# Kernel optimization log

Hardware: AMD Instinct MI355X
Metric: run time of the kernel (lower is better)

The kernel has to match this reference:

```python
import jax, jax.numpy as jnp
import numpy as np

D = 16       # data dimension
M = 64       # hidden width
ALPHA0 = 1.0 # alpha[0]
H_RES = 1.0  # ResNet step h = 1/(n_layers-1), n_layers=2


def _antideriv_tanh(x):
    # log(exp(x)+exp(-x)), numerically stable
    return jnp.abs(x) + jnp.log1p(jnp.exp(-2.0 * jnp.abs(x)))


def _dtanh(x):
    t = jnp.tanh(x)
    return 1.0 - t * t


def grad_and_hessian_trace(s, w, A, b, K0, b0, K1, b1):
    """OT-Flow analytic grad of Phi and trace of Hessian (w.r.t. first d coords).
    s: (n, d+1) = [x; t]. n_layers=2 -> one residual layer, h=1."""
    d = s.shape[1] - 1
    opening = s @ K0.T + b0                         # (n, m)
    u0 = _antideriv_tanh(opening)                   # (n, m)
    feat1 = u0 @ K1.T + b1                          # (n, m)
    tanhopen = jnp.tanh(opening)                    # (n, m)
    # backward pass for gradient: z1 = w + h K1^T (tanh(feat1) * w)
    z1 = w + H_RES * (jnp.tanh(feat1) * w) @ K1     # (n, m)
    z0 = (tanhopen * z1) @ K0                       # (n, d+1)
    symA = A.T @ A                                  # (d+1, d+1)
    grad = z0 + s @ symA + b                        # (n, d+1)
    # Hessian trace: opening-layer term
    Kopen = K0[:, :d]                               # (m, d)
    trH = (_dtanh(opening) * z1) @ jnp.sum(Kopen**2, axis=1)   # (n,)
    # forward-propagated Jacobian of u0 w.r.t. x: (n, m, d)
    Jac = tanhopen[:, :, None] * Kopen[None, :, :]
    KJ = jnp.einsum('ij,njd->nid', K1, Jac)         # (n, m, d)
    t1 = jnp.einsum('nm,nmd->n', _dtanh(feat1) * w, KJ**2)
    trH = trH + H_RES * t1 + jnp.sum(A[:, :d] ** 2)  # + trace(symA[:d,:d])
    return grad, trH


def odefun(z, t, w, A, b, K0, b0, K1, b1):
    n = z.shape[0]
    x = z[:, :D]
    s = jnp.concatenate([x, jnp.full((n, 1), t, dtype=z.dtype)], axis=1)
    gradPhi, trH = grad_and_hessian_trace(s, w, A, b, K0, b0, K1, b1)
    dx = -(1.0 / ALPHA0) * gradPhi[:, :D]
    dl = -(1.0 / ALPHA0) * trH[:, None]
    dv = 0.5 * jnp.sum(dx * dx, axis=1, keepdims=True)
    dr = jnp.abs(-gradPhi[:, -1:] + ALPHA0 * dv)
    return jnp.concatenate([dx, dl, dv, dr], axis=1)


def step_rk4(f, z, t0, t1):
    h = t1 - t0
    z0 = z
    K = h * f(z0, t0)
    z = z0 + K / 6.0
    K = h * f(z0 + 0.5 * K, t0 + 0.5 * h)
    z = z + K / 3.0
    K = h * f(z0 + 0.5 * K, t0 + 0.5 * h)
    z = z + K / 3.0
    K = h * f(z0 + K, t0 + h)
    z = z + K / 6.0
    return z


def setup_inputs() -> dict:
    key = jax.random.key(0)
    ks = jax.random.split(key, 8)
    n = 32768
    dp1 = D + 1
    x = jax.random.normal(ks[0], (n, D), dtype=jnp.float32)
    w = jax.random.normal(ks[1], (M,), dtype=jnp.float32) / np.sqrt(M)
    A = 0.1 * jax.random.normal(ks[2], (10, dp1), dtype=jnp.float32)
    b = 0.1 * jax.random.normal(ks[3], (dp1,), dtype=jnp.float32)
    K0 = jax.random.normal(ks[4], (M, dp1), dtype=jnp.float32) / np.sqrt(dp1)
    b0 = 0.1 * jax.random.normal(ks[5], (M,), dtype=jnp.float32)
    K1 = jax.random.normal(ks[6], (M, M), dtype=jnp.float32) / np.sqrt(M)
    b1 = 0.1 * jax.random.normal(ks[7], (M,), dtype=jnp.float32)
    return {"x": x, "w": w, "A": A, "b": b, "K0": K0, "b0": b0,
            "K1": K1, "b1": b1, "nt": 8}


def reference(x, w, A, b, K0, b0, K1, b1, nt):
    f = lambda z, t: odefun(z, t, w, A, b, K0, b0, K1, b1)
    h = 1.0 / nt
    z = jnp.concatenate([x, jnp.zeros((x.shape[0], 3), x.dtype)], axis=1)
    for k in range(nt):  # nt is a static python int
        z = step_rk4(f, z, k * h, (k + 1) * h)
    # unpack: (x_latent, log_det, transport_cost, hjb_violation)
    return z[:, :D], z[:, D], z[:, D + 1], z[:, D + 2]
```

## Files before the change

### kernel.cpp

```cpp
#include <hip/hip_runtime.h>
#include <math.h>

typedef __attribute__((ext_vector_type(8))) short bf16x8;
typedef __attribute__((ext_vector_type(4))) float f32x4;
typedef __attribute__((ext_vector_type(2))) float f32x2;
typedef __attribute__((ext_vector_type(4))) unsigned u32x4;

union B8 { bf16x8 v; unsigned u[4]; u32x4 q; };

__device__ __forceinline__ unsigned pk2(float lo, float hi) {
  unsigned r;
  asm("v_cvt_pk_bf16_f32 %0, %1, %2" : "=v"(r) : "v"(lo), "v"(hi));
  return r;
}
__device__ __forceinline__ f32x2 pkmul(f32x2 a, f32x2 b) {
  f32x2 r;
  asm("v_pk_mul_f32 %0, %1, %2" : "=v"(r) : "v"(a), "v"(b));
  return r;
}
__device__ __forceinline__ float rcpf(float x) { return __builtin_amdgcn_rcpf(x); }
__device__ __forceinline__ void ldsfence() { asm volatile("s_waitcnt lgkmcnt(0)" ::: "memory"); }

#define MFMA __builtin_amdgcn_mfma_f32_16x16x32_bf16

__global__ void otflow_prep(const float* __restrict__ K0g,
                            const float* __restrict__ Ag,
                            float* __restrict__ ws) {
  __shared__ float Als[170];
  int tid = threadIdx.x;
  for (int idx = tid; idx < 1024; idx += 256) {
    int m = idx >> 4, d = idx & 15;
    ws[idx] = K0g[m * 17 + d];
  }
  if (tid < 170) Als[tid] = Ag[tid];
  if (tid < 64) {
    float s = 0.f;
    for (int d = 0; d < 16; ++d) { float v = K0g[tid * 17 + d]; s += v * v; }
    ws[1320 + tid] = s;
  }
  __syncthreads();
  for (int idx = tid; idx < 289; idx += 256) {
    int j = idx / 17, k2 = idx % 17;
    float s = 0.f;
#pragma unroll
    for (int r = 0; r < 10; ++r) s += Als[r * 17 + j] * Als[r * 17 + k2];
    ws[1024 + idx] = s;
  }
  __syncthreads();
  if (tid == 0) {
    float s = 0.f;
    for (int r = 0; r < 10; ++r)
      for (int j = 0; j < 16; ++j) { float v = Als[r * 17 + j]; s += v * v; }
    ws[1313] = s;
  }
}

__global__ __launch_bounds__(64, 2) void otflow_main(
    const float* __restrict__ xg, const float* __restrict__ wg,
    const float* __restrict__ bg, const float* __restrict__ K0g,
    const float* __restrict__ b0g, const float* __restrict__ K1g,
    const float* __restrict__ b1g, const int* __restrict__ ntg,
    const float* __restrict__ ws, float* __restrict__ out, int n) {
  __shared__ __align__(16) float csh[16 * 68];
  __shared__ __align__(16) float qsh[16 * 68];
  __shared__ __align__(16) unsigned Xu[16 * 36];
  __shared__ __align__(16) float tsh[16 * 20];
  __shared__ __align__(16) float b0s[64], tcs[64], b1s[64], wss[64], k0qs[64];
  __shared__ __align__(16) float scol[20];

  const int lane = threadIdx.x;
  const int lr = lane & 15;
  const int lg = lane >> 4;

  b0s[lane] = b0g[lane];
  tcs[lane] = K0g[lane * 17 + 16];
  b1s[lane] = b1g[lane];
  wss[lane] = wg[lane];
  k0qs[lane] = ws[1320 + lane];
  if (lane < 17) scol[lane] = ws[1024 + lane * 17 + 16];
  if (lane == 17) scol[17] = bg[16];

  const float sumA2 = ws[1313];

  B8 aK0[4], aK0L[4];
#pragma unroll
  for (int mi = 0; mi < 4; ++mi) {
    B8 th, tl;
#pragma unroll
    for (int jj = 0; jj < 4; ++jj) {
      float e0 = K0g[(mi * 16 + lr) * 17 + (lg & 1) * 8 + jj * 2];
      float e1 = K0g[(mi * 16 + lr) * 17 + (lg & 1) * 8 + jj * 2 + 1];
      unsigned hh = pk2(e0, e1);
      th.u[jj] = hh;
      float l0 = e0 - __uint_as_float(hh << 16);
      float l1 = e1 - __uint_as_float(hh & 0xffff0000u);
      tl.u[jj] = pk2(l0, l1);
    }
    aK0[mi] = th; aK0L[mi] = tl;
  }
  B8 aK1[8];
#pragma unroll
  for (int mi = 0; mi < 4; ++mi)
#pragma unroll
    for (int kb = 0; kb < 2; ++kb) {
      const float* pp = K1g + (mi * 16 + lr) * 64 + kb * 32 + lg * 8;
      float4 q0 = *(const float4*)pp;
      float4 q1 = *(const float4*)(pp + 4);
      B8 t;
      t.u[0] = pk2(q0.x, q0.y); t.u[1] = pk2(q0.z, q0.w);
      t.u[2] = pk2(q1.x, q1.y); t.u[3] = pk2(q1.z, q1.w);
      aK1[mi * 2 + kb] = t;
    }
  B8 aK1T[8];
#pragma unroll
  for (int mi = 0; mi < 4; ++mi)
#pragma unroll
    for (int kb = 0; kb < 2; ++kb) {
      int ib = kb * 32 + lg * 8;
      int m = mi * 16 + lr;
      B8 tt;
#pragma unroll
      for (int jj = 0; jj < 4; ++jj)
        tt.u[jj] = pk2(K1g[(ib + jj * 2) * 64 + m], K1g[(ib + jj * 2 + 1) * 64 + m]);
      aK1T[mi * 2 + kb] = tt;
    }
  B8 aG0[3];
  {
    int j = lr;
#pragma unroll
    for (int kb = 0; kb < 3; ++kb) {
      float e[8];
#pragma unroll
      for (int jj = 0; jj < 8; ++jj) {
        float v;
        if (kb < 2) v = K0g[(kb * 32 + lg * 8 + jj) * 17 + j];
        else {
          int kr = lg * 8 + jj;
          v = (kr < 17) ? ws[1024 + kr * 17 + j] : (kr == 17) ? bg[j] : 0.f;
        }
        e[jj] = v;
      }
      B8 t;
      t.u[0] = pk2(e[0], e[1]); t.u[1] = pk2(e[2], e[3]);
      t.u[2] = pk2(e[4], e[5]); t.u[3] = pk2(e[6], e[7]);
      aG0[kb] = t;
    }
  }
  f32x2 kop2[8];
#pragma unroll
  for (int kb = 0; kb < 2; ++kb)
#pragma unroll
    for (int j = 0; j < 4; ++j) {
      f32x2 t;
      t.x = ws[(kb * 32 + lg * 8 + 2 * j) * 16 + lr];
      t.y = ws[(kb * 32 + lg * 8 + 2 * j + 1) * 16 + lr];
      kop2[kb * 4 + j] = t;
    }

  ldsfence();

  float4 sc4 = *(const float4*)(scol + lg * 4);
  const float sc16 = scol[16], sc17 = scol[17];

  const int nt = *ntg;
  const float h = 1.0f / (float)nt;
  const int p0 = blockIdx.x * 16;
  int pidx = p0 + lr; if (pidx >= n) pidx = n - 1;

  float xin[4], x0s[4], xac[4];
  {
    float4 xi = *(const float4*)(xg + (size_t)pidx * 16 + lg * 4);
    xin[0] = xi.x; xin[1] = xi.y; xin[2] = xi.z; xin[3] = xi.w;
#pragma unroll
    for (int r = 0; r < 4; ++r) { x0s[r] = xin[r]; xac[r] = xin[r]; }
  }
  float lacc = 0.f, vacc = 0.f, racc = 0.f;
  const f32x4 zz = {0.f, 0.f, 0.f, 0.f};

  for (int kstep = 0; kstep < nt; ++kstep) {
    float t0 = (float)kstep * h;
#pragma unroll 1
    for (int st = 0; st < 4; ++st) {
      float tin = t0 + ((st == 0) ? 0.f : (st == 3) ? h : 0.5f * h);

      { float4 xv = {xin[0], xin[1], xin[2], xin[3]};
        *(float4*)(csh + lr * 68 + lg * 4) = xv; }
      ldsfence();
      float4 s0 = *(const float4*)(csh + lr * 68 + (lg & 1) * 8);
      float4 s1 = *(const float4*)(csh + lr * 68 + (lg & 1) * 8 + 4);
      unsigned h0 = pk2(s0.x, s0.y), h1 = pk2(s0.z, s0.w);
      unsigned h2 = pk2(s1.x, s1.y), h3 = pk2(s1.z, s1.w);
      B8 sfO, sfG;
      if (lg < 2) {
        sfO.u[0] = h0; sfO.u[1] = h1; sfO.u[2] = h2; sfO.u[3] = h3;
        sfG.u[0] = h0; sfG.u[1] = h1; sfG.u[2] = h2; sfG.u[3] = h3;
      } else {
        float l0 = s0.x - __uint_as_float(h0 << 16);
        float l1 = s0.y - __uint_as_float(h0 & 0xffff0000u);
        float l2 = s0.z - __uint_as_float(h1 << 16);
        float l3 = s0.w - __uint_as_float(h1 & 0xffff0000u);
        float l4 = s1.x - __uint_as_float(h2 << 16);
        float l5 = s1.y - __uint_as_float(h2 & 0xffff0000u);
        float l6 = s1.z - __uint_as_float(h3 << 16);
        float l7 = s1.w - __uint_as_float(h3 & 0xffff0000u);
        sfO.u[0] = pk2(l0, l1); sfO.u[1] = pk2(l2, l3);
        sfO.u[2] = pk2(l4, l5); sfO.u[3] = pk2(l6, l7);
        if (lg == 2) { sfG.u[0] = pk2(tin, 1.f); sfG.u[1] = 0; sfG.u[2] = 0; sfG.u[3] = 0; }
        else { sfG.u[0] = 0; sfG.u[1] = 0; sfG.u[2] = 0; sfG.u[3] = 0; }
      }

      f32x4 o0 = MFMA(aK0[0].v, sfO.v, zz, 0, 0, 0);
      f32x4 o1 = MFMA(aK0[1].v, sfO.v, zz, 0, 0, 0);
      f32x4 o2 = MFMA(aK0[2].v, sfO.v, zz, 0, 0, 0);
      f32x4 o3 = MFMA(aK0[3].v, sfO.v, zz, 0, 0, 0);
      o0 = MFMA(aK0L[0].v, sfO.v, o0, 0, 0, 0);
      o1 = MFMA(aK0L[1].v, sfO.v, o1, 0, 0, 0);
      o2 = MFMA(aK0L[2].v, sfO.v, o2, 0, 0, 0);
      o3 = MFMA(aK0L[3].v, sfO.v, o3, 0, 0, 0);

      float cva[16];
#pragma unroll
      for (int mi = 0; mi < 4; ++mi) {
        f32x4 oa = (mi == 0) ? o0 : (mi == 1) ? o1 : (mi == 2) ? o2 : o3;
        float4 b0v = *(const float4*)(b0s + mi * 16 + lg * 4);
        float4 tcv = *(const float4*)(tcs + mi * 16 + lg * 4);
        float u0v[4];
        float4 cv4;
#pragma unroll
        for (int r = 0; r < 4; ++r) {
          float ov = oa[r] + fmaf(tin, ((const float*)&tcv)[r], ((const float*)&b0v)[r]);
          float e = __expf(-2.f * fabsf(ov));
          float rp = rcpf(1.f + e);
          float c = __builtin_copysignf((1.f - e) * rp, ov);
          cva[mi * 4 + r] = c;
          u0v[r] = fabsf(ov) + __logf(1.f + e);
          ((float*)&cv4)[r] = c;
        }
        *(float4*)(csh + lr * 68 + mi * 16 + lg * 4) = cv4;
        *(uint2*)(Xu + lr * 36 + mi * 8 + lg * 2) =
            make_uint2(pk2(u0v[0], u0v[1]), pk2(u0v[2], u0v[3]));
      }
      ldsfence();

      B8 uf0, uf1;
      uf0.q = *(const u32x4*)(Xu + lr * 36 + lg * 4);
      uf1.q = *(const u32x4*)(Xu + lr * 36 + 16 + lg * 4);
      f32x4 f0 = MFMA(aK1[0].v, uf0.v, zz, 0, 0, 0); f0 = MFMA(aK1[1].v, uf1.v, f0, 0, 0, 0);
      f32x4 f1 = MFMA(aK1[2].v, uf0.v, zz, 0, 0, 0); f1 = MFMA(aK1[3].v, uf1.v, f1, 0, 0, 0);
      f32x4 f2 = MFMA(aK1[4].v, uf0.v, zz, 0, 0, 0); f2 = MFMA(aK1[5].v, uf1.v, f2, 0, 0, 0);
      f32x4 f3 = MFMA(aK1[6].v, uf0.v, zz, 0, 0, 0); f3 = MFMA(aK1[7].v, uf1.v, f3, 0, 0, 0);

#pragma unroll
      for (int mi = 0; mi < 4; ++mi) {
        f32x4 fa = (mi == 0) ? f0 : (mi == 1) ? f1 : (mi == 2) ? f2 : f3;
        float4 b1v = *(const float4*)(b1s + mi * 16 + lg * 4);
        float4 wv = *(const float4*)(wss + mi * 16 + lg * 4);
        float av[4];
        float4 qv4;
#pragma unroll
        for (int r = 0; r < 4; ++r) {
          float fv = fa[r] + ((const float*)&b1v)[r];
          float e = __expf(-2.f * fabsf(fv));
          float rp = rcpf(1.f + e);
          float tf = __builtin_copysignf((1.f - e) * rp, fv);
          float wr = ((const float*)&wv)[r];
          av[r] = tf * wr;
          ((float*)&qv4)[r] = (1.f - tf * tf) * wr;
        }
        *(float4*)(qsh + lr * 68 + mi * 16 + lg * 4) = qv4;
        *(uint2*)(Xu + lr * 36 + mi * 8 + lg * 2) =
            make_uint2(pk2(av[0], av[1]), pk2(av[2], av[3]));
      }
      ldsfence();

      B8 af0, af1;
      af0.q = *(const u32x4*)(Xu + lr * 36 + lg * 4);
      af1.q = *(const u32x4*)(Xu + lr * 36 + 16 + lg * 4);
      f32x4 z0 = MFMA(aK1T[0].v, af0.v, zz, 0, 0, 0); z0 = MFMA(aK1T[1].v, af1.v, z0, 0, 0, 0);
      f32x4 z1 = MFMA(aK1T[2].v, af0.v, zz, 0, 0, 0); z1 = MFMA(aK1T[3].v, af1.v, z1, 0, 0, 0);
      f32x4 z2 = MFMA(aK1T[4].v, af0.v, zz, 0, 0, 0); z2 = MFMA(aK1T[5].v, af1.v, z2, 0, 0, 0);
      f32x4 z3 = MFMA(aK1T[6].v, af0.v, zz, 0, 0, 0); z3 = MFMA(aK1T[7].v, af1.v, z3, 0, 0, 0);

      float trh_l = 0.f, g16p = 0.f;
#pragma unroll
      for (int mi = 0; mi < 4; ++mi) {
        f32x4 za = (mi == 0) ? z0 : (mi == 1) ? z1 : (mi == 2) ? z2 : z3;
        float4 wv = *(const float4*)(wss + mi * 16 + lg * 4);
        float4 kq = *(const float4*)(k0qs + mi * 16 + lg * 4);
        float4 tcv = *(const float4*)(tcs + mi * 16 + lg * 4);
        float rv[4];
#pragma unroll
        for (int r = 0; r < 4; ++r) {
          float c = cva[mi * 4 + r];
          float z1v = za[r] + ((const float*)&wv)[r];
          rv[r] = c * z1v;
          trh_l = fmaf((1.f - c * c) * z1v, ((const float*)&kq)[r], trh_l);
          g16p = fmaf(rv[r], ((const float*)&tcv)[r], g16p);
        }
        *(uint2*)(Xu + lr * 36 + mi * 8 + lg * 2) =
            make_uint2(pk2(rv[0], rv[1]), pk2(rv[2], rv[3]));
      }
#pragma unroll
      for (int r = 0; r < 4; ++r) g16p = fmaf(xin[r], ((const float*)&sc4)[r], g16p);
      trh_l += __shfl_xor(trh_l, 16, 64);
      trh_l += __shfl_xor(trh_l, 32, 64);
      g16p += __shfl_xor(g16p, 16, 64);
      g16p += __shfl_xor(g16p, 32, 64);
      float g16 = g16p + fmaf(tin, sc16, sc17);
      ldsfence();

#pragma unroll 2
      for (int p = 0; p < 16; ++p) {
        const float* cp = csh + p * 68;
        float4 ca = *(const float4*)(cp + lg * 8);
        float4 cb = *(const float4*)(cp + lg * 8 + 4);
        float4 cc = *(const float4*)(cp + 32 + lg * 8);
        float4 cd = *(const float4*)(cp + 32 + lg * 8 + 4);
        B8 y0, y1;
        f32x2 pr;
        pr = pkmul((f32x2){ca.x, ca.y}, kop2[0]); y0.u[0] = pk2(pr.x, pr.y);
        pr = pkmul((f32x2){ca.z, ca.w}, kop2[1]); y0.u[1] = pk2(pr.x, pr.y);
        pr = pkmul((f32x2){cb.x, cb.y}, kop2[2]); y0.u[2] = pk2(pr.x, pr.y);
        pr = pkmul((f32x2){cb.z, cb.w}, kop2[3]); y0.u[3] = pk2(pr.x, pr.y);
        pr = pkmul((f32x2){cc.x, cc.y}, kop2[4]); y1.u[0] = pk2(pr.x, pr.y);
        pr = pkmul((f32x2){cc.z, cc.w}, kop2[5]); y1.u[1] = pk2(pr.x, pr.y);
        pr = pkmul((f32x2){cd.x, cd.y}, kop2[6]); y1.u[2] = pk2(pr.x, pr.y);
        pr = pkmul((f32x2){cd.z, cd.w}, kop2[7]); y1.u[3] = pk2(pr.x, pr.y);
        f32x4 kc0 = MFMA(y0.v, aK1[0].v, zz, 0, 0, 0); kc0 = MFMA(y1.v, aK1[1].v, kc0, 0, 0, 0);
        f32x4 kc1 = MFMA(y0.v, aK1[2].v, zz, 0, 0, 0); kc1 = MFMA(y1.v, aK1[3].v, kc1, 0, 0, 0);
        f32x4 kc2 = MFMA(y0.v, aK1[4].v, zz, 0, 0, 0); kc2 = MFMA(y1.v, aK1[5].v, kc2, 0, 0, 0);
        f32x4 kc3 = MFMA(y0.v, aK1[6].v, zz, 0, 0, 0); kc3 = MFMA(y1.v, aK1[7].v, kc3, 0, 0, 0);
        float q0 = qsh[p * 68 + lr];
        float q1 = qsh[p * 68 + 16 + lr];
        float q2 = qsh[p * 68 + 32 + lr];
        float q3 = qsh[p * 68 + 48 + lr];
        float d0 = kc0[0] * kc0[0] + kc0[1] * kc0[1] + kc0[2] * kc0[2] + kc0[3] * kc0[3];
        float d1 = kc1[0] * kc1[0] + kc1[1] * kc1[1] + kc1[2] * kc1[2] + kc1[3] * kc1[3];
        float d2 = kc2[0] * kc2[0] + kc2[1] * kc2[1] + kc2[2] * kc2[2] + kc2[3] * kc2[3];
        float d3 = kc3[0] * kc3[0] + kc3[1] * kc3[1] + kc3[2] * kc3[2] + kc3[3] * kc3[3];
        float tp = q0 * d0 + q1 * d1 + q2 * d2 + q3 * d3;
        tp += __shfl_xor(tp, 16, 64);
        tp += __shfl_xor(tp, 32, 64);
        if (lg == 0) tsh[p * 20 + lr] = tp;
      }

      B8 rf0, rf1;
      rf0.q = *(const u32x4*)(Xu + lr * 36 + lg * 4);
      rf1.q = *(const u32x4*)(Xu + lr * 36 + 16 + lg * 4);
      f32x4 g0 = MFMA(aG0[0].v, rf0.v, zz, 0, 0, 0);
      g0 = MFMA(aG0[1].v, rf1.v, g0, 0, 0, 0);
      g0 = MFMA(aG0[2].v, sfG.v, g0, 0, 0, 0);
      ldsfence();

      float4 tv = *(const float4*)(tsh + lr * 20 + lg * 4);
      float tsum = tv.x + tv.y + tv.z + tv.w;
      tsum += __shfl_xor(tsum, 16, 64);
      tsum += __shfl_xor(tsum, 32, 64);

      float kx[4];
      float dvp = 0.f;
#pragma unroll
      for (int r = 0; r < 4; ++r) { float d = -g0[r]; kx[r] = d; dvp = fmaf(d, d, dvp); }
      dvp += __shfl_xor(dvp, 16, 64);
      dvp += __shfl_xor(dvp, 32, 64);
      dvp *= 0.5f;
      float trH = trh_l + tsum + sumA2;
      float dl = -trH;
      float dr = fabsf(dvp - g16);
      float wch = ((st == 0 || st == 3) ? (1.f / 6.f) : (1.f / 3.f)) * h;
#pragma unroll
      for (int r = 0; r < 4; ++r) xac[r] = fmaf(wch, kx[r], xac[r]);
      lacc = fmaf(wch, dl, lacc);
      vacc = fmaf(wch, dvp, vacc);
      racc = fmaf(wch, dr, racc);
      if (st < 3) {
        float anh = ((st == 2) ? 1.f : 0.5f) * h;
#pragma unroll
        for (int r = 0; r < 4; ++r) xin[r] = fmaf(anh, kx[r], x0s[r]);
      } else {
#pragma unroll
        for (int r = 0; r < 4; ++r) { x0s[r] = xac[r]; xin[r] = xac[r]; }
      }
    }
  }

  if (p0 + lr < n) {
    float4 xa = {xac[0], xac[1], xac[2], xac[3]};
    *(float4*)(out + (size_t)(p0 + lr) * 16 + lg * 4) = xa;
    if (lg == 0) {
      out[(size_t)n * 16 + p0 + lr] = lacc;
      out[(size_t)n * 17 + p0 + lr] = vacc;
      out[(size_t)n * 18 + p0 + lr] = racc;
    }
  }
}

extern "C" void kernel_launch(void* const* d_in, const int* in_sizes, int n_in,
                              void* d_out, int out_size, void* d_ws, size_t ws_size,
                              hipStream_t stream) {
  const float* xg = (const float*)d_in[0];
  const float* wg = (const float*)d_in[1];
  const float* Ag = (const float*)d_in[2];
  const float* bg = (const float*)d_in[3];
  const float* K0g = (const float*)d_in[4];
  const float* b0g = (const float*)d_in[5];
  const float* K1g = (const float*)d_in[6];
  const float* b1g = (const float*)d_in[7];
  const int* ntg = (const int*)d_in[8];
  float* out = (float*)d_out;
  float* ws = (float*)d_ws;
  int n = in_sizes[0] / 16;

  hipLaunchKernelGGL(otflow_prep, dim3(1), dim3(256), 0, stream, K0g, Ag, ws);
  int nblk = (n + 15) / 16;
  hipLaunchKernelGGL(otflow_main, dim3(nblk), dim3(64), 0, stream,
                     xg, wg, bg, K0g, b0g, K1g, b1g, ntg, ws, out, n);
}
```

Measured before the change: 349.5 us.

## Process eight points per wave and split tile rows across half-waves

Each 64-lane block now handles 8 points instead of 16. The two half-groups of 16 lanes (lr<8 and lr>=8) duplicate the point columns in the MFMA B operand and split the four m-tiles of elementwise tanh/log work between them. Partial Hessian-trace and gradient sums are combined with an extra xor-8 shuffle, and the per-point second-order loop shrinks to 8 iterations. The grid doubles, which gives more waves per SIMD to hide the serial latency chain. The cost is half of each MFMA's columns doing redundant work.

After: 386.3 us. 1.11x slower.

```diff
diff --git a/kernel.cpp b/kernel.cpp
--- a/kernel.cpp
+++ b/kernel.cpp
@@ -61,16 +61,18 @@
     const float* __restrict__ b0g, const float* __restrict__ K1g,
     const float* __restrict__ b1g, const int* __restrict__ ntg,
     const float* __restrict__ ws, float* __restrict__ out, int n) {
-  __shared__ __align__(16) float csh[16 * 68];
-  __shared__ __align__(16) float qsh[16 * 68];
-  __shared__ __align__(16) unsigned Xu[16 * 36];
-  __shared__ __align__(16) float tsh[16 * 20];
+  __shared__ __align__(16) float csh[8 * 68];
+  __shared__ __align__(16) float qsh[8 * 68];
+  __shared__ __align__(16) unsigned Xu[8 * 36];
+  __shared__ __align__(16) float tsh[8 * 20];
   __shared__ __align__(16) float b0s[64], tcs[64], b1s[64], wss[64], k0qs[64];
   __shared__ __align__(16) float scol[20];
 
   const int lane = threadIdx.x;
   const int lr = lane & 15;
   const int lg = lane >> 4;
+  const int p8 = lr & 7;
+  const int mh = (lr >> 3) << 1;
 
   b0s[lane] = b0g[lane];
   tcs[lane] = K0g[lane * 17 + 16];
@@ -164,8 +166,8 @@
 
   const int nt = *ntg;
   const float h = 1.0f / (float)nt;
-  const int p0 = blockIdx.x * 16;
-  int pidx = p0 + lr; if (pidx >= n) pidx = n - 1;
+  const int p0 = blockIdx.x * 8;
+  int pidx = p0 + p8; if (pidx >= n) pidx = n - 1;
 
   float xin[4], x0s[4], xac[4];
   {
@@ -183,11 +185,13 @@
     for (int st = 0; st < 4; ++st) {
       float tin = t0 + ((st == 0) ? 0.f : (st == 3) ? h : 0.5f * h);
 
-      { float4 xv = {xin[0], xin[1], xin[2], xin[3]};
-        *(float4*)(csh + lr * 68 + lg * 4) = xv; }
+      if (lr < 8) {
+        float4 xv = {xin[0], xin[1], xin[2], xin[3]};
+        *(float4*)(csh + p8 * 68 + lg * 4) = xv;
+      }
       ldsfence();
-      float4 s0 = *(const float4*)(csh + lr * 68 + (lg & 1) * 8);
-      float4 s1 = *(const float4*)(csh + lr * 68 + (lg & 1) * 8 + 4);
+      float4 s0 = *(const float4*)(csh + p8 * 68 + (lg & 1) * 8);
+      float4 s1 = *(const float4*)(csh + p8 * 68 + (lg & 1) * 8 + 4);
       unsigned h0 = pk2(s0.x, s0.y), h1 = pk2(s0.z, s0.w);
       unsigned h2 = pk2(s1.x, s1.y), h3 = pk2(s1.z, s1.w);
       B8 sfO, sfG;
@@ -218,9 +222,10 @@
       o2 = MFMA(aK0L[2].v, sfO.v, o2, 0, 0, 0);
       o3 = MFMA(aK0L[3].v, sfO.v, o3, 0, 0, 0);
 
-      float cva[16];
-#pragma unroll
-      for (int mi = 0; mi < 4; ++mi) {
+      float cva[8];
+#pragma unroll
+      for (int t = 0; t < 2; ++t) {
+        int mi = mh + t;
         f32x4 oa = (mi == 0) ? o0 : (mi == 1) ? o1 : (mi == 2) ? o2 : o3;
         float4 b0v = *(const float4*)(b0s + mi * 16 + lg * 4);
         float4 tcv = *(const float4*)(tcs + mi * 16 + lg * 4);
@@ -232,26 +237,27 @@
           float e = __expf(-2.f * fabsf(ov));
           float rp = rcpf(1.f + e);
           float c = __builtin_copysignf((1.f - e) * rp, ov);
-          cva[mi * 4 + r] = c;
+          cva[t * 4 + r] = c;
           u0v[r] = fabsf(ov) + __logf(1.f + e);
           ((float*)&cv4)[r] = c;
         }
-        *(float4*)(csh + lr * 68 + mi * 16 + lg * 4) = cv4;
-        *(uint2*)(Xu + lr * 36 + mi * 8 + lg * 2) =
+        *(float4*)(csh + p8 * 68 + mi * 16 + lg * 4) = cv4;
+        *(uint2*)(Xu + p8 * 36 + mi * 8 + lg * 2) =
             make_uint2(pk2(u0v[0], u0v[1]), pk2(u0v[2], u0v[3]));
       }
       ldsfence();
 
       B8 uf0, uf1;
-      uf0.q = *(const u32x4*)(Xu + lr * 36 + lg * 4);
-      uf1.q = *(const u32x4*)(Xu + lr * 36 + 16 + lg * 4);
+      uf0.q = *(const u32x4*)(Xu + p8 * 36 + lg * 4);
+      uf1.q = *(const u32x4*)(Xu + p8 * 36 + 16 + lg * 4);
       f32x4 f0 = MFMA(aK1[0].v, uf0.v, zz, 0, 0, 0); f0 = MFMA(aK1[1].v, uf1.v, f0, 0, 0, 0);
       f32x4 f1 = MFMA(aK1[2].v, uf0.v, zz, 0, 0, 0); f1 = MFMA(aK1[3].v, uf1.v, f1, 0, 0, 0);
       f32x4 f2 = MFMA(aK1[4].v, uf0.v, zz, 0, 0, 0); f2 = MFMA(aK1[5].v, uf1.v, f2, 0, 0, 0);
       f32x4 f3 = MFMA(aK1[6].v, uf0.v, zz, 0, 0, 0); f3 = MFMA(aK1[7].v, uf1.v, f3, 0, 0, 0);
 
 #pragma unroll
-      for (int mi = 0; mi < 4; ++mi) {
+      for (int t = 0; t < 2; ++t) {
+        int mi = mh + t;
         f32x4 fa = (mi == 0) ? f0 : (mi == 1) ? f1 : (mi == 2) ? f2 : f3;
         float4 b1v = *(const float4*)(b1s + mi * 16 + lg * 4);
         float4 wv = *(const float4*)(wss + mi * 16 + lg * 4);
@@ -267,15 +273,15 @@
           av[r] = tf * wr;
           ((float*)&qv4)[r] = (1.f - tf * tf) * wr;
         }
-        *(float4*)(qsh + lr * 68 + mi * 16 + lg * 4) = qv4;
-        *(uint2*)(Xu + lr * 36 + mi * 8 + lg * 2) =
+        *(float4*)(qsh + p8 * 68 + mi * 16 + lg * 4) = qv4;
+        *(uint2*)(Xu + p8 * 36 + mi * 8 + lg * 2) =
             make_uint2(pk2(av[0], av[1]), pk2(av[2], av[3]));
       }
       ldsfence();
 
       B8 af0, af1;
-      af0.q = *(const u32x4*)(Xu + lr * 36 + lg * 4);
-      af1.q = *(const u32x4*)(Xu + lr * 36 + 16 + lg * 4);
+      af0.q = *(const u32x4*)(Xu + p8 * 36 + lg * 4);
+      af1.q = *(const u32x4*)(Xu + p8 * 36 + 16 + lg * 4);
       f32x4 z0 = MFMA(aK1T[0].v, af0.v, zz, 0, 0, 0); z0 = MFMA(aK1T[1].v, af1.v, z0, 0, 0, 0);
       f32x4 z1 = MFMA(aK1T[2].v, af0.v, zz, 0, 0, 0); z1 = MFMA(aK1T[3].v, af1.v, z1, 0, 0, 0);
       f32x4 z2 = MFMA(aK1T[4].v, af0.v, zz, 0, 0, 0); z2 = MFMA(aK1T[5].v, af1.v, z2, 0, 0, 0);
@@ -283,7 +289,8 @@
 
       float trh_l = 0.f, g16p = 0.f;
 #pragma unroll
-      for (int mi = 0; mi < 4; ++mi) {
+      for (int t = 0; t < 2; ++t) {
+        int mi = mh + t;
         f32x4 za = (mi == 0) ? z0 : (mi == 1) ? z1 : (mi == 2) ? z2 : z3;
         float4 wv = *(const float4*)(wss + mi * 16 + lg * 4);
         float4 kq = *(const float4*)(k0qs + mi * 16 + lg * 4);
@@ -291,26 +298,30 @@
         float rv[4];
 #pragma unroll
         for (int r = 0; r < 4; ++r) {
-          float c = cva[mi * 4 + r];
+          float c = cva[t * 4 + r];
           float z1v = za[r] + ((const float*)&wv)[r];
           rv[r] = c * z1v;
           trh_l = fmaf((1.f - c * c) * z1v, ((const float*)&kq)[r], trh_l);
           g16p = fmaf(rv[r], ((const float*)&tcv)[r], g16p);
         }
-        *(uint2*)(Xu + lr * 36 + mi * 8 + lg * 2) =
+        *(uint2*)(Xu + p8 * 36 + mi * 8 + lg * 2) =
             make_uint2(pk2(rv[0], rv[1]), pk2(rv[2], rv[3]));
       }
-#pragma unroll
-      for (int r = 0; r < 4; ++r) g16p = fmaf(xin[r], ((const float*)&sc4)[r], g16p);
+      if (lr < 8) {
+#pragma unroll
+        for (int r = 0; r < 4; ++r) g16p = fmaf(xin[r], ((const float*)&sc4)[r], g16p);
+      }
+      trh_l += __shfl_xor(trh_l, 8, 64);
       trh_l += __shfl_xor(trh_l, 16, 64);
       trh_l += __shfl_xor(trh_l, 32, 64);
+      g16p += __shfl_xor(g16p, 8, 64);
       g16p += __shfl_xor(g16p, 16, 64);
       g16p += __shfl_xor(g16p, 32, 64);
       float g16 = g16p + fmaf(tin, sc16, sc17);
       ldsfence();
 
 #pragma unroll 2
-      for (int p = 0; p < 16; ++p) {
+      for (int p = 0; p < 8; ++p) {
         const float* cp = csh + p * 68;
         float4 ca = *(const float4*)(cp + lg * 8);
         float4 cb = *(const float4*)(cp + lg * 8 + 4);
@@ -345,14 +356,14 @@
       }
 
       B8 rf0, rf1;
-      rf0.q = *(const u32x4*)(Xu + lr * 36 + lg * 4);
-      rf1.q = *(const u32x4*)(Xu + lr * 36 + 16 + lg * 4);
+      rf0.q = *(const u32x4*)(Xu + p8 * 36 + lg * 4);
+      rf1.q = *(const u32x4*)(Xu + p8 * 36 + 16 + lg * 4);
       f32x4 g0 = MFMA(aG0[0].v, rf0.v, zz, 0, 0, 0);
       g0 = MFMA(aG0[1].v, rf1.v, g0, 0, 0, 0);
       g0 = MFMA(aG0[2].v, sfG.v, g0, 0, 0, 0);
       ldsfence();
 
-      float4 tv = *(const float4*)(tsh + lr * 20 + lg * 4);
+      float4 tv = *(const float4*)(tsh + p8 * 20 + lg * 4);
       float tsum = tv.x + tv.y + tv.z + tv.w;
       tsum += __shfl_xor(tsum, 16, 64);
       tsum += __shfl_xor(tsum, 32, 64);
@@ -384,13 +395,13 @@
     }
   }
 
-  if (p0 + lr < n) {
+  if (lr < 8 && p0 + p8 < n) {
     float4 xa = {xac[0], xac[1], xac[2], xac[3]};
-    *(float4*)(out + (size_t)(p0 + lr) * 16 + lg * 4) = xa;
+    *(float4*)(out + (size_t)(p0 + p8) * 16 + lg * 4) = xa;
     if (lg == 0) {
-      out[(size_t)n * 16 + p0 + lr] = lacc;
-      out[(size_t)n * 17 + p0 + lr] = vacc;
-      out[(size_t)n * 18 + p0 + lr] = racc;
+      out[(size_t)n * 16 + p0 + p8] = lacc;
+      out[(size_t)n * 17 + p0 + p8] = vacc;
+      out[(size_t)n * 18 + p0 + p8] = racc;
     }
   }
 }
@@ -412,7 +423,7 @@
   int n = in_sizes[0] / 16;
 
   hipLaunchKernelGGL(otflow_prep, dim3(1), dim3(256), 0, stream, K0g, Ag, ws);
-  int nblk = (n + 15) / 16;
+  int nblk = (n + 7) / 8;
   hipLaunchKernelGGL(otflow_main, dim3(nblk), dim3(64), 0, stream,
                      xg, wg, bg, K0g, b0g, K1g, b1g, ntg, ws, out, n);
 }
```
